# Performance work log

Measured on AMD Instinct MI355X. Metric: run time of the kernel, lower is better.

Reference implementation:

```python
import jax, jax.numpy as jnp
import numpy as np

H = 12        # attention heads
BETA = 0.5    # blend weight between ctx-cosine probs and QK probs
LN_EPS = 1e-12


def layer_norm(x, g, b):
    mu = x.mean(-1, keepdims=True)
    var = ((x - mu) ** 2).mean(-1, keepdims=True)
    return (x - mu) * jax.lax.rsqrt(var + LN_EPS) * g + b


def setup_inputs() -> dict:
    key = jax.random.key(0)
    B, S, D, F, L = 16, 512, 768, 3072, 4
    ks = jax.random.split(key, 9)
    w = lambda k, shape: (jax.random.normal(k, shape, jnp.float32) * 0.02)
    return {
        "hidden_states": jax.random.normal(ks[0], (B, S, D), jnp.float32),
        "Wq": w(ks[1], (L, D, D)), "bq": jnp.zeros((L, D), jnp.float32),
        "Wk": w(ks[2], (L, D, D)), "bk": jnp.zeros((L, D), jnp.float32),
        "Wv": w(ks[3], (L, D, D)), "bv": jnp.zeros((L, D), jnp.float32),
        "Wc": w(ks[4], (L, D, D)), "bc": jnp.zeros((L, D), jnp.float32),
        "Wo": w(ks[5], (L, D, D)), "bo": jnp.zeros((L, D), jnp.float32),
        "g1": jnp.ones((L, D), jnp.float32), "b1": jnp.zeros((L, D), jnp.float32),
        "Wi": w(ks[6], (L, D, F)), "bi": jnp.zeros((L, F), jnp.float32),
        "Wo2": w(ks[7], (L, F, D)), "bo2": jnp.zeros((L, D), jnp.float32),
        "g2": jnp.ones((L, D), jnp.float32), "b2": jnp.zeros((L, D), jnp.float32),
    }


def reference(hidden_states, Wq, bq, Wk, bk, Wv, bv, Wc, bc, Wo, bo,
              g1, b1, Wi, bi, Wo2, bo2, g2, b2):
    B, S, D = hidden_states.shape
    Dh = D // H
    L = Wq.shape[0]
    eye = jnp.eye(S, dtype=hidden_states.dtype)
    scale = 1.0 / np.sqrt(Dh).astype(np.float32)

    def heads(t):  # [B,S,D] -> [B,H,S,Dh]
        return t.reshape(B, S, H, Dh).transpose(0, 2, 1, 3)

    x = hidden_states
    for i in range(L):  # small fixed layer loop
        q = heads(x @ Wq[i] + bq[i])
        k = heads(x @ Wk[i] + bk[i])
        v = heads(x @ Wv[i] + bv[i])
        c = heads(x @ Wc[i] + bc[i])

        # Branch 1: cosine-normalized context scores, flipped (1 - cos) + I
        cn = jnp.linalg.norm(c, axis=-1, keepdims=True)           # [B,H,S,1]
        denom = cn * jnp.swapaxes(cn, -1, -2)                     # [B,H,S,S]
        s1 = 1.0 - jnp.einsum('bhld,bhrd->bhlr', c, c) / denom + eye
        p1 = jax.nn.softmax(s1, axis=-1)

        # Branch 2: standard scaled QK scores
        s2 = jnp.einsum('bhld,bhrd->bhlr', q, k) * scale
        p2 = jax.nn.softmax(s2, axis=-1)

        p = BETA * p1 + (1.0 - BETA) * p2                          # beta blend
        ctx = jnp.einsum('bhlr,bhrd->bhld', p, v)                  # [B,H,S,Dh]
        ctx = ctx.transpose(0, 2, 1, 3).reshape(B, S, D)

        attn_out = layer_norm(ctx @ Wo[i] + bo[i] + x, g1[i], b1[i])
        h = jax.nn.gelu(attn_out @ Wi[i] + bi[i], approximate=False)
        x = layer_norm(h @ Wo2[i] + bo2[i] + attn_out, g2[i], b2[i])
    return x
```

## Files before the change

kernel.cpp:

```cpp
#include <hip/hip_runtime.h>
#include <math.h>

#define DD 768
#define FF 3072
#define SS 512
#define BB 16
#define NH 12
#define DH 64
#define NL 4
#define MM (BB*SS)

typedef __attribute__((ext_vector_type(8))) short short8;
typedef __attribute__((ext_vector_type(4))) float f32x4;

__device__ __forceinline__ unsigned short f2bf(float f) {
  unsigned u = __float_as_uint(f);
  return (unsigned short)((u + 0x7FFFu + ((u >> 16) & 1u)) >> 16);
}
__device__ __forceinline__ float bf2f(unsigned short s) {
  return __uint_as_float(((unsigned)s) << 16);
}

#define GLOAD_LDS(g, l) \
  __builtin_amdgcn_global_load_lds((const __attribute__((address_space(1))) void*)(g), \
                                   (__attribute__((address_space(3))) void*)(l), 16, 0, 0)

__global__ __launch_bounds__(256) void cvt_dual_k(const float* __restrict__ in,
                                                  float* __restrict__ outf,
                                                  unsigned short* __restrict__ outb, int n) {
  for (int i = blockIdx.x*256 + threadIdx.x; i < n; i += gridDim.x*256) {
    float v = in[i]; outf[i] = v; outb[i] = f2bf(v);
  }
}

__global__ __launch_bounds__(256) void tcvt_k(const float* __restrict__ src,
                                              unsigned short* __restrict__ dst,
                                              int K, int N) {
  __shared__ float t[32][33];
  const int n0 = blockIdx.x*32, k0 = blockIdx.y*32;
  const int tx = threadIdx.x & 31, ty = threadIdx.x >> 5;
#pragma unroll
  for (int i = 0; i < 32; i += 8)
    t[ty+i][tx] = src[(size_t)(k0+ty+i)*N + n0+tx];
  __syncthreads();
#pragma unroll
  for (int i = 0; i < 32; i += 8)
    dst[(size_t)(n0+ty+i)*K + k0+tx] = f2bf(t[tx][ty+i]);
}

__global__ __launch_bounds__(256) void bcat_k(const float* __restrict__ a,
                                              const float* __restrict__ b,
                                              const float* __restrict__ c,
                                              const float* __restrict__ d,
                                              float* __restrict__ out) {
  int i = blockIdx.x*256 + threadIdx.x;
  int w = i / 768;
  const float* s = (w == 0) ? a : (w == 1) ? b : (w == 2) ? c : d;
  out[i] = s[i - w*768];
}

template<int EPI, int OBF>
__global__ __launch_bounds__(256) void mgemm_k(
    const unsigned short* __restrict__ A,
    const unsigned short* __restrict__ Bw,
    const float* __restrict__ bias,
    const float* __restrict__ resid,
    void* __restrict__ Cout, int M, int N, int K)
{
  __shared__ __align__(16) unsigned short As[128*32];
  __shared__ __align__(16) unsigned short Bs[128*32];
  const int nwg = gridDim.x * gridDim.y;
  int lin = blockIdx.y * gridDim.x + blockIdx.x;
  lin = (lin & 7) * (nwg >> 3) + (lin >> 3);
  const int bm = (lin / gridDim.x) * 128, bn = (lin % gridDim.x) * 128;
  const int tid = threadIdx.x;
  const int wave = tid >> 6, lane = tid & 63;
  const int wm = (wave >> 1)*64, wn = (wave & 1)*64;

  f32x4 acc[4][4] = {};

  const unsigned short* Ag = A  + (size_t)(bm + wave*32 + (lane>>2))*K + (lane&3)*8;
  const unsigned short* Bg = Bw + (size_t)(bn + wave*32 + (lane>>2))*K + (lane&3)*8;
  unsigned short* AsW = As + wave*32*32;
  unsigned short* BsW = Bs + wave*32*32;

  for (int k0 = 0; k0 < K; k0 += 32) {
    GLOAD_LDS(Ag,                AsW);
    GLOAD_LDS(Ag + 16*(size_t)K, AsW + 16*32);
    GLOAD_LDS(Bg,                BsW);
    GLOAD_LDS(Bg + 16*(size_t)K, BsW + 16*32);
    Ag += 32; Bg += 32;
    __syncthreads();
    short8 af[4], bfr[4];
#pragma unroll
    for (int i = 0; i < 4; ++i) {
      af[i]  = *(const short8*)&As[(wm + i*16 + (lane & 15))*32 + (lane >> 4)*8];
      bfr[i] = *(const short8*)&Bs[(wn + i*16 + (lane & 15))*32 + (lane >> 4)*8];
    }
#pragma unroll
    for (int i = 0; i < 4; ++i)
#pragma unroll
      for (int j = 0; j < 4; ++j)
        acc[i][j] = __builtin_amdgcn_mfma_f32_16x16x32_bf16(af[i], bfr[j], acc[i][j], 0, 0, 0);
    __syncthreads();
  }

  const int col0 = bn + wn + (lane & 15);
  const int row0 = bm + wm + (lane >> 4)*4;
#pragma unroll
  for (int i = 0; i < 4; ++i) {
#pragma unroll
    for (int j = 0; j < 4; ++j) {
      const int n = col0 + j*16;
      const float bv = bias[n];
#pragma unroll
      for (int r = 0; r < 4; ++r) {
        const int m = row0 + i*16 + r;
        float v = acc[i][j][r] + bv;
        if (EPI == 1) v += resid[(size_t)m*N + n];
        if (EPI == 2) v = 0.5f*v*(1.0f + erff(v*0.70710678118654752f));
        if (OBF) ((unsigned short*)Cout)[(size_t)m*N + n] = f2bf(v);
        else     ((float*)Cout)[(size_t)m*N + n] = v;
      }
    }
  }
}

__global__ __launch_bounds__(256) void cnorm_k(const unsigned short* __restrict__ c,
                                               float* __restrict__ rn) {
  int idx = blockIdx.x*4 + (threadIdx.x >> 6);
  int lane = threadIdx.x & 63;
  int s  = idx % SS;
  int bh = idx / SS;
  int h  = bh % NH;
  int b  = bh / NH;
  float v = bf2f(c[((size_t)(b*SS + s))*FF + h*DH + lane]);
  float ss = v*v;
#pragma unroll
  for (int off = 32; off; off >>= 1) ss += __shfl_xor(ss, off, 64);
  if (lane == 0) rn[idx] = rsqrtf(ss);
}

__global__ __launch_bounds__(256) void vtrans_k(const unsigned short* __restrict__ v,
                                                unsigned short* __restrict__ VT) {
  __shared__ unsigned short t[64][72];
  const int s0 = blockIdx.x*64;
  const int h  = blockIdx.y;
  const int b  = blockIdx.z;
  const size_t base = (size_t)(b*SS)*FF + h*DH;
  const int row = threadIdx.x >> 2, seg = threadIdx.x & 3;
  const unsigned short* vg = v + base + (size_t)(s0+row)*FF + seg*16;
  *(uint4*)&t[row][seg*16]     = *(const uint4*)vg;
  *(uint4*)&t[row][seg*16 + 8] = *(const uint4*)(vg + 8);
  __syncthreads();
  unsigned short o[16];
#pragma unroll
  for (int u = 0; u < 16; ++u) o[u] = t[seg*16 + u][row];
  unsigned short* og = VT + ((size_t)(b*NH + h)*DH + row)*SS + s0 + seg*16;
  *(uint4*)og       = *(const uint4*)&o[0];
  *(uint4*)(og + 8) = *(const uint4*)&o[8];
}

__global__ __launch_bounds__(256, 3) void attn5_k(
    const unsigned short* __restrict__ q, const unsigned short* __restrict__ k,
    const unsigned short* __restrict__ c, const float* __restrict__ rn,
    const unsigned short* __restrict__ VT, unsigned short* __restrict__ ctxO)
{
  const int bid = blockIdx.x + 8*blockIdx.y + 96*blockIdx.z;
  const int l0  = ((bid >> 3) & 7) << 6;
  const int bh  = (bid & 7) + ((bid >> 6) << 3);
  const int h   = bh % NH;
  const int b   = bh / NH;
  const int tid = threadIdx.x;
  const int wave = tid >> 6, lane = tid & 63;
  const int wm = wave * 16;
  const int fr = lane & 15;
  const int fg = lane >> 4;
  const size_t base   = (size_t)(b*SS)*FF + h*DH;
  const size_t vtbase = (size_t)bh*DH*SS;

  __shared__ __align__(16) unsigned short Ks [2][64*72];
  __shared__ __align__(16) unsigned short Crs[2][64*72];
  __shared__ __align__(16) unsigned short Ps [4][16*72];
  unsigned short* Pw = Ps[wave];

  const unsigned short* qrow = q + base + (size_t)(l0 + wm + fr)*FF + fg*8;
  const unsigned short* crow = c + base + (size_t)(l0 + wm + fr)*FF + fg*8;
  const short8 aQ0 = *(const short8*)qrow;
  const short8 aQ1 = *(const short8*)(qrow + 32);
  const short8 aC0 = *(const short8*)crow;
  const short8 aC1 = *(const short8*)(crow + 32);

  float rnl[4];
#pragma unroll
  for (int reg = 0; reg < 4; ++reg)
    rnl[reg] = rn[(size_t)bh*SS + l0 + wm + fg*4 + reg];

  const int srow = tid >> 2, sseg = tid & 3;
  {
    const unsigned short* kg = k + base + (size_t)srow*FF + sseg*16;
    const unsigned short* cg = c + base + (size_t)srow*FF + sseg*16;
    *(uint4*)&Ks [0][srow*72 + sseg*16]     = *(const uint4*)kg;
    *(uint4*)&Ks [0][srow*72 + sseg*16 + 8] = *(const uint4*)(kg + 8);
    *(uint4*)&Crs[0][srow*72 + sseg*16]     = *(const uint4*)cg;
    *(uint4*)&Crs[0][srow*72 + sseg*16 + 8] = *(const uint4*)(cg + 8);
  }
  __syncthreads();

  float rs2[4], rs1[4];
#pragma unroll
  for (int r = 0; r < 4; ++r) { rs2[r] = 0.f; rs1[r] = 0.f; }
  f32x4 oc1[4] = {}, oc2[4] = {};

#pragma unroll 1
  for (int it = 0; it < 8; ++it) {
    const int r0 = it*64;
    const int cur = it & 1, nxt = cur ^ 1;

    uint4 nk0, nk1, nc0, nc1;
    if (it < 7) {
      const unsigned short* kg = k + base + (size_t)(r0 + 64 + srow)*FF + sseg*16;
      const unsigned short* cg = c + base + (size_t)(r0 + 64 + srow)*FF + sseg*16;
      nk0 = *(const uint4*)kg;  nk1 = *(const uint4*)(kg + 8);
      nc0 = *(const uint4*)cg;  nc1 = *(const uint4*)(cg + 8);
    }

    float rnr[4];
    short8 bv0[4], bv1[4];
#pragma unroll
    for (int nt = 0; nt < 4; ++nt) {
      rnr[nt] = rn[(size_t)bh*SS + r0 + nt*16 + fr];
      const unsigned short* vtr = VT + vtbase + (size_t)(nt*16 + fr)*SS + r0 + fg*8;
      bv0[nt] = *(const short8*)vtr;
      bv1[nt] = *(const short8*)(vtr + 32);
    }

    f32x4 s1a[4] = {}, s2a[4] = {};
#pragma unroll
    for (int nt = 0; nt < 4; ++nt) {
      const short8 bK0 = *(const short8*)&Ks [cur][(nt*16+fr)*72 + fg*8];
      const short8 bK1 = *(const short8*)&Ks [cur][(nt*16+fr)*72 + fg*8 + 32];
      const short8 bC0 = *(const short8*)&Crs[cur][(nt*16+fr)*72 + fg*8];
      const short8 bC1 = *(const short8*)&Crs[cur][(nt*16+fr)*72 + fg*8 + 32];
      s2a[nt] = __builtin_amdgcn_mfma_f32_16x16x32_bf16(aQ0, bK0, s2a[nt], 0,0,0);
      s2a[nt] = __builtin_amdgcn_mfma_f32_16x16x32_bf16(aQ1, bK1, s2a[nt], 0,0,0);
      s1a[nt] = __builtin_amdgcn_mfma_f32_16x16x32_bf16(aC0, bC0, s1a[nt], 0,0,0);
      s1a[nt] = __builtin_amdgcn_mfma_f32_16x16x32_bf16(aC1, bC1, s1a[nt], 0,0,0);
    }

    float sv1[4][4], sv2[4][4];
#pragma unroll
    for (int nt = 0; nt < 4; ++nt)
#pragma unroll
      for (int reg = 0; reg < 4; ++reg) {
        const int ql = wm + fg*4 + reg;
        const int rr = nt*16 + fr;
        sv2[reg][nt] = s2a[nt][reg] * 0.125f;
        sv1[reg][nt] = 1.0f - s1a[nt][reg]*rnl[reg]*rnr[nt]
                     + ((l0+ql) == (r0+rr) ? 1.0f : 0.0f);
      }

#pragma unroll
    for (int reg = 0; reg < 4; ++reg) {
      const int prow = (fg*4 + reg)*72;
#pragma unroll
      for (int nt = 0; nt < 4; ++nt) {
        const float x1 = __expf(sv1[reg][nt] - 3.0f);
        Pw[prow + nt*16 + fr] = f2bf(x1);
        rs1[reg] += x1;
      }
    }
    {
      const short8 p0 = *(const short8*)&Pw[fr*72 + fg*8];
      const short8 p1 = *(const short8*)&Pw[fr*72 + fg*8 + 32];
#pragma unroll
      for (int nt = 0; nt < 4; ++nt) {
        oc1[nt] = __builtin_amdgcn_mfma_f32_16x16x32_bf16(p0, bv0[nt], oc1[nt], 0,0,0);
        oc1[nt] = __builtin_amdgcn_mfma_f32_16x16x32_bf16(p1, bv1[nt], oc1[nt], 0,0,0);
      }
    }

#pragma unroll
    for (int reg = 0; reg < 4; ++reg) {
      const int prow = (fg*4 + reg)*72;
#pragma unroll
      for (int nt = 0; nt < 4; ++nt) {
        const float x2 = __expf(sv2[reg][nt] - 3.0f);
        Pw[prow + nt*16 + fr] = f2bf(x2);
        rs2[reg] += x2;
      }
    }
    {
      const short8 p0 = *(const short8*)&Pw[fr*72 + fg*8];
      const short8 p1 = *(const short8*)&Pw[fr*72 + fg*8 + 32];
#pragma unroll
      for (int nt = 0; nt < 4; ++nt) {
        oc2[nt] = __builtin_amdgcn_mfma_f32_16x16x32_bf16(p0, bv0[nt], oc2[nt], 0,0,0);
        oc2[nt] = __builtin_amdgcn_mfma_f32_16x16x32_bf16(p1, bv1[nt], oc2[nt], 0,0,0);
      }
    }

    if (it < 7) {
      *(uint4*)&Ks [nxt][srow*72 + sseg*16]     = nk0;
      *(uint4*)&Ks [nxt][srow*72 + sseg*16 + 8] = nk1;
      *(uint4*)&Crs[nxt][srow*72 + sseg*16]     = nc0;
      *(uint4*)&Crs[nxt][srow*72 + sseg*16 + 8] = nc1;
    }
    __syncthreads();
  }

#pragma unroll
  for (int reg = 0; reg < 4; ++reg) {
    float t1 = rs1[reg], t2 = rs2[reg];
#pragma unroll
    for (int off = 1; off < 16; off <<= 1) {
      t1 += __shfl_xor(t1, off, 64);
      t2 += __shfl_xor(t2, off, 64);
    }
    const float i1 = 0.5f / t1;
    const float i2 = 0.5f / t2;
    const int prow = (fg*4 + reg)*72;
#pragma unroll
    for (int nt = 0; nt < 4; ++nt)
      Pw[prow + nt*16 + fr] = f2bf(oc1[nt][reg]*i1 + oc2[nt][reg]*i2);
  }
  {
    const int row = lane >> 2, seg = lane & 3;
    const int Mrow = b*SS + l0 + wm + row;
    unsigned short* og = ctxO + (size_t)Mrow*DD + h*DH + seg*16;
    *(uint4*)og       = *(const uint4*)&Pw[row*72 + seg*16];
    *(uint4*)(og + 8) = *(const uint4*)&Pw[row*72 + seg*16 + 8];
  }
}

__global__ __launch_bounds__(256) void ln_k(const float* __restrict__ in,
                                            const float* __restrict__ g,
                                            const float* __restrict__ b,
                                            float* __restrict__ outf,
                                            unsigned short* __restrict__ outb) {
  __shared__ float xs[DD];
  __shared__ float red[4];
  const int tid = threadIdx.x;
  const float* xr = in + (size_t)blockIdx.x * DD;
  float* xo = outf + (size_t)blockIdx.x * DD;
  unsigned short* xbr = outb + (size_t)blockIdx.x * DD;
  float s = 0.f;
  for (int d = tid; d < DD; d += 256) { float v = xr[d]; xs[d] = v; s += v; }
#pragma unroll
  for (int off = 32; off; off >>= 1) s += __shfl_xor(s, off, 64);
  if ((tid & 63) == 0) red[tid >> 6] = s;
  __syncthreads();
  float mu = (red[0]+red[1]+red[2]+red[3]) * (1.f/DD);
  __syncthreads();
  float s2 = 0.f;
  for (int d = tid; d < DD; d += 256) { float t = xs[d]-mu; s2 += t*t; }
#pragma unroll
  for (int off = 32; off; off >>= 1) s2 += __shfl_xor(s2, off, 64);
  if ((tid & 63) == 0) red[tid >> 6] = s2;
  __syncthreads();
  float var = (red[0]+red[1]+red[2]+red[3]) * (1.f/DD);
  float rstd = rsqrtf(var + 1e-12f);
  for (int d = tid; d < DD; d += 256) {
    float o = (xs[d]-mu)*rstd*g[d] + b[d];
    xo[d] = o;
    xbr[d] = f2bf(o);
  }
}

extern "C" void kernel_launch(void* const* d_in, const int* in_sizes, int n_in,
                              void* d_out, int out_size, void* d_ws, size_t ws_size,
                              hipStream_t stream) {
  const float* hs  = (const float*)d_in[0];
  const float* Wq  = (const float*)d_in[1];  const float* bq  = (const float*)d_in[2];
  const float* Wk  = (const float*)d_in[3];  const float* bk  = (const float*)d_in[4];
  const float* Wv  = (const float*)d_in[5];  const float* bv  = (const float*)d_in[6];
  const float* Wc  = (const float*)d_in[7];  const float* bc  = (const float*)d_in[8];
  const float* Wo  = (const float*)d_in[9];  const float* bo  = (const float*)d_in[10];
  const float* g1  = (const float*)d_in[11]; const float* b1  = (const float*)d_in[12];
  const float* Wi  = (const float*)d_in[13]; const float* bi  = (const float*)d_in[14];
  const float* Wo2 = (const float*)d_in[15]; const float* bo2 = (const float*)d_in[16];
  const float* g2  = (const float*)d_in[17]; const float* b2  = (const float*)d_in[18];

  const size_t XN  = (size_t)MM * DD;
  const size_t HN  = (size_t)MM * FF;
  const int    nBH = BB*NH*SS;
  const size_t WTN = 7667712;

  char* p = (char*)d_ws;
  float*          x      = (float*)p;           p += XN*4;
  float*          attnf  = (float*)p;           p += XN*4;
  unsigned short* qkvc16 = (unsigned short*)p;  p += HN*2;
  unsigned short* xb16   = (unsigned short*)p;  p += XN*2;
  unsigned short* ctx16  = (unsigned short*)p;  p += XN*2;
  unsigned short* attn16 = (unsigned short*)p;  p += XN*2;
  unsigned short* vt16   = (unsigned short*)p;  p += XN*2;
  unsigned short* WT     = (unsigned short*)p;  p += WTN*2;
  float*          bqkvc  = (float*)p;           p += 3072*4;
  float*          cnb    = (float*)p;           p += (size_t)nBH*4;
  const size_t need = (size_t)(p - (char*)d_ws);
  if (ws_size < need) return;

  unsigned short* WqkvcT = WT;
  unsigned short* WoT    = WT + 2359296;
  unsigned short* WiT    = WT + 2949120;
  unsigned short* Wo2T   = WT + 5308416;
  unsigned short* hb16   = qkvc16;

  cvt_dual_k<<<4096, 256, 0, stream>>>(hs, x, xb16, (int)XN);

  dim3 gGQ(FF/128, MM/128);
  dim3 gGD(DD/128, MM/128);
  dim3 gA(SS/64, NH, BB);
  dim3 tDD(DD/32, DD/32);
  dim3 tDF(FF/32, DD/32);
  dim3 tFD(DD/32, FF/32);

  for (int i = 0; i < NL; ++i) {
    const size_t wD = (size_t)i*DD*DD, wF = (size_t)i*DD*FF;
    tcvt_k<<<tDD, 256, 0, stream>>>(Wq + wD, WqkvcT,            DD, DD);
    tcvt_k<<<tDD, 256, 0, stream>>>(Wk + wD, WqkvcT +  768*768, DD, DD);
    tcvt_k<<<tDD, 256, 0, stream>>>(Wv + wD, WqkvcT + 1536*768, DD, DD);
    tcvt_k<<<tDD, 256, 0, stream>>>(Wc + wD, WqkvcT + 2304*768, DD, DD);
    tcvt_k<<<tDD, 256, 0, stream>>>(Wo + wD, WoT,  DD, DD);
    tcvt_k<<<tDF, 256, 0, stream>>>(Wi + wF, WiT,  DD, FF);
    tcvt_k<<<tFD, 256, 0, stream>>>(Wo2 + wF, Wo2T, FF, DD);
    bcat_k<<<12, 256, 0, stream>>>(bq + (size_t)i*DD, bk + (size_t)i*DD,
                                   bv + (size_t)i*DD, bc + (size_t)i*DD, bqkvc);

    mgemm_k<0,1><<<gGQ, 256, 0, stream>>>(xb16, WqkvcT, bqkvc, nullptr, qkvc16, MM, FF, DD);

    cnorm_k<<<nBH/4, 256, 0, stream>>>(qkvc16 + 2304, cnb);
    vtrans_k<<<gA, 256, 0, stream>>>(qkvc16 + 1536, vt16);
    attn5_k<<<gA, 256, 0, stream>>>(qkvc16, qkvc16 + 768, qkvc16 + 2304,
                                    cnb, vt16, ctx16);

    mgemm_k<1,0><<<gGD, 256, 0, stream>>>(ctx16, WoT, bo + (size_t)i*DD, x, attnf, MM, DD, DD);
    ln_k<<<MM, 256, 0, stream>>>(attnf, g1 + (size_t)i*DD, b1 + (size_t)i*DD, attnf, attn16);

    mgemm_k<2,1><<<gGQ, 256, 0, stream>>>(attn16, WiT, bi + (size_t)i*FF, nullptr, hb16, MM, FF, DD);
    mgemm_k<1,0><<<gGD, 256, 0, stream>>>(hb16, Wo2T, bo2 + (size_t)i*DD, attnf, x, MM, DD, FF);
    float* lnout = (i == NL-1) ? (float*)d_out : x;
    ln_k<<<MM, 256, 0, stream>>>(x, g2 + (size_t)i*DD, b2 + (size_t)i*DD, lnout, xb16);
  }
}
```

Before: 1.604 ms.

## Double-buffer LDS tiles in GEMM to overlap global loads with MFMA

```diff
diff --git a/kernel.cpp b/kernel.cpp
--- a/kernel.cpp
+++ b/kernel.cpp
@@ -60,15 +60,15 @@
 }
 
 template<int EPI, int OBF>
-__global__ __launch_bounds__(256) void mgemm_k(
+__global__ __launch_bounds__(256, 3) void mgemm_k(
     const unsigned short* __restrict__ A,
     const unsigned short* __restrict__ Bw,
     const float* __restrict__ bias,
     const float* __restrict__ resid,
     void* __restrict__ Cout, int M, int N, int K)
 {
-  __shared__ __align__(16) unsigned short As[128*32];
-  __shared__ __align__(16) unsigned short Bs[128*32];
+  __shared__ __align__(16) unsigned short As[2][128*32];
+  __shared__ __align__(16) unsigned short Bs[2][128*32];
   const int nwg = gridDim.x * gridDim.y;
   int lin = blockIdx.y * gridDim.x + blockIdx.x;
   lin = (lin & 7) * (nwg >> 3) + (lin >> 3);
@@ -76,33 +76,63 @@
   const int tid = threadIdx.x;
   const int wave = tid >> 6, lane = tid & 63;
   const int wm = (wave >> 1)*64, wn = (wave & 1)*64;
+  const int woff = wave*32*32;
 
   f32x4 acc[4][4] = {};
 
   const unsigned short* Ag = A  + (size_t)(bm + wave*32 + (lane>>2))*K + (lane&3)*8;
   const unsigned short* Bg = Bw + (size_t)(bn + wave*32 + (lane>>2))*K + (lane&3)*8;
-  unsigned short* AsW = As + wave*32*32;
-  unsigned short* BsW = Bs + wave*32*32;
-
-  for (int k0 = 0; k0 < K; k0 += 32) {
-    GLOAD_LDS(Ag,                AsW);
-    GLOAD_LDS(Ag + 16*(size_t)K, AsW + 16*32);
-    GLOAD_LDS(Bg,                BsW);
-    GLOAD_LDS(Bg + 16*(size_t)K, BsW + 16*32);
+
+  GLOAD_LDS(Ag,                As[0] + woff);
+  GLOAD_LDS(Ag + 16*(size_t)K, As[0] + woff + 16*32);
+  GLOAD_LDS(Bg,                Bs[0] + woff);
+  GLOAD_LDS(Bg + 16*(size_t)K, Bs[0] + woff + 16*32);
+  Ag += 32; Bg += 32;
+  __syncthreads();
+
+  const unsigned short* Ac = As[0]; unsigned short* An = As[1];
+  const unsigned short* Bc = Bs[0]; unsigned short* Bn = Bs[1];
+  const int nk = K >> 5;
+
+#pragma unroll 1
+  for (int t = 0; t < nk - 1; ++t) {
+    GLOAD_LDS(Ag,                An + woff);
+    GLOAD_LDS(Ag + 16*(size_t)K, An + woff + 16*32);
+    GLOAD_LDS(Bg,                Bn + woff);
+    GLOAD_LDS(Bg + 16*(size_t)K, Bn + woff + 16*32);
     Ag += 32; Bg += 32;
-    __syncthreads();
+
     short8 af[4], bfr[4];
 #pragma unroll
     for (int i = 0; i < 4; ++i) {
-      af[i]  = *(const short8*)&As[(wm + i*16 + (lane & 15))*32 + (lane >> 4)*8];
-      bfr[i] = *(const short8*)&Bs[(wn + i*16 + (lane & 15))*32 + (lane >> 4)*8];
-    }
+      af[i]  = *(const short8*)&Ac[(wm + i*16 + (lane & 15))*32 + (lane >> 4)*8];
+      bfr[i] = *(const short8*)&Bc[(wn + i*16 + (lane & 15))*32 + (lane >> 4)*8];
+    }
+    __builtin_amdgcn_s_setprio(1);
 #pragma unroll
     for (int i = 0; i < 4; ++i)
 #pragma unroll
       for (int j = 0; j < 4; ++j)
         acc[i][j] = __builtin_amdgcn_mfma_f32_16x16x32_bf16(af[i], bfr[j], acc[i][j], 0, 0, 0);
+    __builtin_amdgcn_s_setprio(0);
+
     __syncthreads();
+    const unsigned short* tA = Ac; Ac = An; An = (unsigned short*)tA;
+    const unsigned short* tB = Bc; Bc = Bn; Bn = (unsigned short*)tB;
+  }
+
+  {
+    short8 af[4], bfr[4];
+#pragma unroll
+    for (int i = 0; i < 4; ++i) {
+      af[i]  = *(const short8*)&Ac[(wm + i*16 + (lane & 15))*32 + (lane >> 4)*8];
+      bfr[i] = *(const short8*)&Bc[(wn + i*16 + (lane & 15))*32 + (lane >> 4)*8];
+    }
+#pragma unroll
+    for (int i = 0; i < 4; ++i)
+#pragma unroll
+      for (int j = 0; j < 4; ++j)
+        acc[i][j] = __builtin_amdgcn_mfma_f32_16x16x32_bf16(af[i], bfr[j], acc[i][j], 0, 0, 0);
   }
 
   const int col0 = bn + wn + (lane & 15);
```

Result: faster. 1.474 ms (-8.1%).

## Triple-buffer GEMM LDS tiles with async prefetch and XOR swizzle

Applied to the files above, without the earlier changes.

```diff
diff --git a/kernel.cpp b/kernel.cpp
--- a/kernel.cpp
+++ b/kernel.cpp
@@ -60,15 +60,15 @@
 }
 
 template<int EPI, int OBF>
-__global__ __launch_bounds__(256) void mgemm_k(
+__global__ __launch_bounds__(256, 3) void mgemm_k(
     const unsigned short* __restrict__ A,
     const unsigned short* __restrict__ Bw,
     const float* __restrict__ bias,
     const float* __restrict__ resid,
     void* __restrict__ Cout, int M, int N, int K)
 {
-  __shared__ __align__(16) unsigned short As[128*32];
-  __shared__ __align__(16) unsigned short Bs[128*32];
+  __shared__ __align__(16) unsigned short As[3][128*32];
+  __shared__ __align__(16) unsigned short Bs[3][128*32];
   const int nwg = gridDim.x * gridDim.y;
   int lin = blockIdx.y * gridDim.x + blockIdx.x;
   lin = (lin & 7) * (nwg >> 3) + (lin >> 3);
@@ -76,34 +76,67 @@
   const int tid = threadIdx.x;
   const int wave = tid >> 6, lane = tid & 63;
   const int wm = (wave >> 1)*64, wn = (wave & 1)*64;
+  const int woff = wave*32*32;
 
   f32x4 acc[4][4] = {};
 
-  const unsigned short* Ag = A  + (size_t)(bm + wave*32 + (lane>>2))*K + (lane&3)*8;
-  const unsigned short* Bg = Bw + (size_t)(bn + wave*32 + (lane>>2))*K + (lane&3)*8;
-  unsigned short* AsW = As + wave*32*32;
-  unsigned short* BsW = Bs + wave*32*32;
-
-  for (int k0 = 0; k0 < K; k0 += 32) {
-    GLOAD_LDS(Ag,                AsW);
-    GLOAD_LDS(Ag + 16*(size_t)K, AsW + 16*32);
-    GLOAD_LDS(Bg,                BsW);
-    GLOAD_LDS(Bg + 16*(size_t)K, BsW + 16*32);
-    Ag += 32; Bg += 32;
-    __syncthreads();
-    short8 af[4], bfr[4];
-#pragma unroll
-    for (int i = 0; i < 4; ++i) {
-      af[i]  = *(const short8*)&As[(wm + i*16 + (lane & 15))*32 + (lane >> 4)*8];
-      bfr[i] = *(const short8*)&Bs[(wn + i*16 + (lane & 15))*32 + (lane >> 4)*8];
-    }
-#pragma unroll
-    for (int i = 0; i < 4; ++i)
-#pragma unroll
-      for (int j = 0; j < 4; ++j)
-        acc[i][j] = __builtin_amdgcn_mfma_f32_16x16x32_bf16(af[i], bfr[j], acc[i][j], 0, 0, 0);
-    __syncthreads();
-  }
+  const int scol = ((lane & 3) ^ ((lane >> 2) & 3)) * 8;
+  const unsigned short* Ag = A  + (size_t)(bm + wave*32 + (lane>>2))*K + scol;
+  const unsigned short* Bg = Bw + (size_t)(bn + wave*32 + (lane>>2))*K + scol;
+
+  unsigned short *aR = As[0], *aM = As[1], *aW = As[2];
+  unsigned short *bR = Bs[0], *bM = Bs[1], *bW = Bs[2];
+  const int nk = K >> 5;
+
+#define MG_STAGE(ad, bd) do { \
+    GLOAD_LDS(Ag,                (ad) + woff); \
+    GLOAD_LDS(Ag + 16*(size_t)K, (ad) + woff + 16*32); \
+    GLOAD_LDS(Bg,                (bd) + woff); \
+    GLOAD_LDS(Bg + 16*(size_t)K, (bd) + woff + 16*32); \
+    Ag += 32; Bg += 32; } while (0)
+
+  const int rdseg = ((lane >> 4) ^ (lane & 3)) * 8;
+#define MG_COMPUTE(as, bs) do { \
+    short8 af[4], bfr[4]; \
+    _Pragma("unroll") \
+    for (int i = 0; i < 4; ++i) { \
+      af[i]  = *(const short8*)&(as)[(wm + i*16 + (lane & 15))*32 + rdseg]; \
+      bfr[i] = *(const short8*)&(bs)[(wn + i*16 + (lane & 15))*32 + rdseg]; \
+    } \
+    __builtin_amdgcn_s_setprio(1); \
+    _Pragma("unroll") \
+    for (int i = 0; i < 4; ++i) \
+      _Pragma("unroll") \
+      for (int j = 0; j < 4; ++j) \
+        acc[i][j] = __builtin_amdgcn_mfma_f32_16x16x32_bf16(af[i], bfr[j], acc[i][j], 0, 0, 0); \
+    __builtin_amdgcn_s_setprio(0); \
+    __builtin_amdgcn_sched_barrier(0); } while (0)
+
+  MG_STAGE(aR, bR);
+  MG_STAGE(aM, bM);
+
+#pragma unroll 1
+  for (int t = 0; t < nk - 2; ++t) {
+    asm volatile("s_waitcnt vmcnt(4)" ::: "memory");
+    __builtin_amdgcn_sched_barrier(0);
+    __builtin_amdgcn_s_barrier();
+    MG_STAGE(aW, bW);
+    MG_COMPUTE(aR, bR);
+    unsigned short* s;
+    s = aR; aR = aM; aM = aW; aW = s;
+    s = bR; bR = bM; bM = bW; bW = s;
+  }
+  asm volatile("s_waitcnt vmcnt(4)" ::: "memory");
+  __builtin_amdgcn_sched_barrier(0);
+  __builtin_amdgcn_s_barrier();
+  MG_COMPUTE(aR, bR);
+  asm volatile("s_waitcnt vmcnt(0)" ::: "memory");
+  __builtin_amdgcn_sched_barrier(0);
+  __builtin_amdgcn_s_barrier();
+  MG_COMPUTE(aM, bM);
+
+#undef MG_STAGE
+#undef MG_COMPUTE
 
   const int col0 = bn + wn + (lane & 15);
   const int row0 = bm + wm + (lane >> 4)*4;
```

Measured after the change: 1.556 ms. -3.0%, faster.
